# Performance work log

Hardware: AMD Instinct MI355X
Metric: run time of the kernel (lower is better)

The kernel has to match this reference:

```python
import jax, jax.numpy as jnp
import numpy as np

B, N, D, H = 2, 4096, 768, 12
HD = D // H  # head_dim = 64


def setup_inputs() -> dict:
    key = jax.random.key(0)
    k1, k2, k3, k4 = jax.random.split(key, 4)
    s = 1.0 / np.sqrt(D)
    return {
        "x": jax.random.normal(k1, (B, N, D), dtype=jnp.float32),
        "W_kqv": jax.random.normal(k2, (H, D, 3 * HD), dtype=jnp.float32) * s,
        "W_proj": jax.random.normal(k3, (D, D), dtype=jnp.float32) * s,
        "b_proj": jax.random.normal(k4, (D,), dtype=jnp.float32) * 0.02,
    }


def reference(x, W_kqv, W_proj, b_proj):
    # Per-head fused KQV projection: [B,N,D] x [H,D,3*HD] -> [B,H,N,3*HD]
    kqv = jnp.einsum("bnd,hde->bhne", x, W_kqv)
    # split order in source: k, q, v
    k, q, v = jnp.split(kqv, 3, axis=-1)  # each [B,H,N,HD]
    scale = 1.0 / np.sqrt(HD)
    scores = jnp.einsum("bhqd,bhkd->bhqk", q, k) * scale  # [B,H,N,N]
    causal = jnp.tril(jnp.ones((N, N), dtype=bool))
    scores = jnp.where(causal, scores, -jnp.inf)
    probs = jax.nn.softmax(scores, axis=-1)
    out = jnp.einsum("bhqk,bhkd->bhqd", probs, v)  # [B,H,N,HD]
    # concat heads along feature dim -> [B,N,D]
    out = out.transpose(0, 2, 1, 3).reshape(B, N, D)
    # output projection (dropout_rate=0.0 -> identity)
    return out @ W_proj.T + b_proj
```

## Files before the change

kernel.cpp:

```cpp
#include <hip/hip_runtime.h>

typedef _Float16 half8 __attribute__((ext_vector_type(8)));
typedef __fp16 fp16x2 __attribute__((ext_vector_type(2)));
typedef float floatx4 __attribute__((ext_vector_type(4)));
typedef float floatx16 __attribute__((ext_vector_type(16)));

#define MFMA_F16(a, b, c) __builtin_amdgcn_mfma_f32_16x16x32_f16((a), (b), (c), 0, 0, 0)
#define MFMA32(a, b, c) __builtin_amdgcn_mfma_f32_32x32x16_f16((a), (b), (c), 0, 0, 0)

__device__ __forceinline__ unsigned short f2h_bits(float f) {
    union { _Float16 h; unsigned short u; } cv;
    cv.h = (_Float16)f;
    return cv.u;
}

__device__ __forceinline__ unsigned pkrtz(float a, float b) {
    union { fp16x2 h; unsigned u; } cv;
    cv.h = __builtin_amdgcn_cvt_pkrtz(a, b);
    return cv.u;
}

__device__ __forceinline__ void swap32(unsigned a, unsigned b, int hi32,
                                       unsigned& r0, unsigned& r1) {
#if __has_builtin(__builtin_amdgcn_permlane32_swap)
    auto r = __builtin_amdgcn_permlane32_swap((int)a, (int)b, false, false);
    r0 = (unsigned)r[0];
    r1 = (unsigned)r[1];
#else
    unsigned ax = (unsigned)__shfl_xor((int)a, 32, 64);
    unsigned bx = (unsigned)__shfl_xor((int)b, 32, 64);
    r0 = hi32 ? bx : a;
    r1 = hi32 ? b : ax;
#endif
}

__device__ __forceinline__ float xhalf_max(float x) {
#if __has_builtin(__builtin_amdgcn_permlane32_swap)
    auto r = __builtin_amdgcn_permlane32_swap(__float_as_int(x), __float_as_int(x), false, false);
    return fmaxf(__int_as_float(r[0]), __int_as_float(r[1]));
#else
    return fmaxf(x, __shfl_xor(x, 32, 64));
#endif
}
__device__ __forceinline__ float xhalf_add(float x) {
#if __has_builtin(__builtin_amdgcn_permlane32_swap)
    auto r = __builtin_amdgcn_permlane32_swap(__float_as_int(x), __float_as_int(x), false, false);
    return __int_as_float(r[0]) + __int_as_float(r[1]);
#else
    return x + __shfl_xor(x, 32, 64);
#endif
}

__global__ void conv_x_kernel(const float* __restrict__ x, unsigned short* __restrict__ xb) {
    int i = blockIdx.x * 256 + threadIdx.x;
    float4 v = ((const float4*)x)[i];
    ushort4 o;
    o.x = f2h_bits(v.x); o.y = f2h_bits(v.y); o.z = f2h_bits(v.z); o.w = f2h_bits(v.w);
    ((ushort4*)xb)[i] = o;
}

__global__ void conv_wkqv_kernel(const float* __restrict__ w, unsigned short* __restrict__ wT) {
    int t = blockIdx.x * 256 + threadIdx.x;
    int d = t % 768;
    int hc = t / 768;
    int h = hc / 192;
    int c = hc - h * 192;
    float v = w[(h * 768 + d) * 192 + c];
    if (c >= 64 && c < 128) v *= 0.18033688011112042f;
    wT[t] = f2h_bits(v);
}

__global__ void conv_wproj_kernel(const float* __restrict__ w, unsigned short* __restrict__ wb) {
    int i = blockIdx.x * 256 + threadIdx.x;
    float4 v = ((const float4*)w)[i];
    ushort4 o;
    o.x = f2h_bits(v.x); o.y = f2h_bits(v.y); o.z = f2h_bits(v.z); o.w = f2h_bits(v.w);
    ((ushort4*)wb)[i] = o;
}

template <int EPI>
__global__ __launch_bounds__(256, 2) void gemm_bt_kernel(
    const unsigned short* __restrict__ A, const unsigned short* __restrict__ Bt,
    unsigned short* __restrict__ o_q, unsigned short* __restrict__ o_k,
    unsigned short* __restrict__ o_vt, float* __restrict__ o_f32,
    const float* __restrict__ bias, int Ntiles) {
    __shared__ unsigned short sA[128 * 64];
    __shared__ unsigned short sB[128 * 64];
    const int tid = threadIdx.x;
    const int lo = tid & 15;
    const int hi = (tid >> 4) & 3;
    const int wid = tid >> 6;
    const int wr = wid >> 1;
    const int wc = wid & 1;
    const int bm = blockIdx.x / Ntiles;
    const int bn = blockIdx.x % Ntiles;
    const size_t rowA0 = (size_t)bm * 128;
    const size_t rowB0 = (size_t)bn * 128;

    const floatx4 ZERO = {0.f, 0.f, 0.f, 0.f};
    floatx4 acc[4][4];
#pragma unroll
    for (int i = 0; i < 4; ++i)
#pragma unroll
        for (int j = 0; j < 4; ++j) acc[i][j] = ZERO;

    const int ldsWaveBase = (tid & 0xC0) << 3;

    for (int kt = 0; kt < 768; kt += 64) {
        __syncthreads();
#pragma unroll
        for (int it = 0; it < 4; ++it) {
            int g = it * 256 + tid;
            int row = g >> 3;
            int slot = g & 7;
            int koff = kt + ((slot ^ (row & 7)) << 3);
            const unsigned short* srcA = A + (rowA0 + row) * 768 + koff;
            const unsigned short* srcB = Bt + (rowB0 + row) * 768 + koff;
            unsigned short* dA = &sA[it * 2048 + ldsWaveBase];
            unsigned short* dB = &sB[it * 2048 + ldsWaveBase];
            __builtin_amdgcn_global_load_lds(
                (const __attribute__((address_space(1))) unsigned int*)srcA,
                (__attribute__((address_space(3))) unsigned int*)dA, 16, 0, 0);
            __builtin_amdgcn_global_load_lds(
                (const __attribute__((address_space(1))) unsigned int*)srcB,
                (__attribute__((address_space(3))) unsigned int*)dB, 16, 0, 0);
        }
        __syncthreads();
#pragma unroll
        for (int kc = 0; kc < 2; ++kc) {
            half8 av[4], bv[4];
#pragma unroll
            for (int mi = 0; mi < 4; ++mi) {
                int row = wr * 64 + mi * 16 + lo;
                av[mi] = *(const half8*)&sA[row * 64 + (((kc * 4 + hi) ^ (lo & 7)) << 3)];
            }
#pragma unroll
            for (int ni = 0; ni < 4; ++ni) {
                int row = wc * 64 + ni * 16 + lo;
                bv[ni] = *(const half8*)&sB[row * 64 + (((kc * 4 + hi) ^ (lo & 7)) << 3)];
            }
#pragma unroll
            for (int mi = 0; mi < 4; ++mi)
#pragma unroll
                for (int ni = 0; ni < 4; ++ni)
                    acc[mi][ni] = MFMA_F16(av[mi], bv[ni], acc[mi][ni]);
        }
    }

    if (EPI == 0) {
#pragma unroll
        for (int ni = 0; ni < 4; ++ni) {
            int gn = (int)rowB0 + wc * 64 + ni * 16 + lo;
            unsigned h = (unsigned)gn / 192u;
            int c = gn - (int)h * 192;
#pragma unroll
            for (int mi = 0; mi < 4; ++mi) {
#pragma unroll
                for (int r = 0; r < 4; ++r) {
                    int gm = (int)rowA0 + wr * 64 + mi * 16 + hi * 4 + r;
                    int b = gm >> 12;
                    int n = gm & 4095;
                    int bh = b * 12 + (int)h;
                    unsigned short val = f2h_bits(acc[mi][ni][r]);
                    if (c < 64) {
                        int t = n >> 5;
                        size_t idx = ((((size_t)bh * 128 + t) * 4 + (c >> 4)) * 64 +
                                      (((c >> 3) & 1) * 32 + (n & 31))) * 8 + (c & 7);
                        o_k[idx] = val;
                    } else if (c < 128) {
                        int d = c - 64;
                        int t = n >> 5;
                        size_t idx = ((((size_t)bh * 128 + t) * 4 + (d >> 4)) * 64 +
                                      (((d >> 3) & 1) * 32 + (n & 31))) * 8 + (d & 7);
                        o_q[idx] = val;
                    } else {
                        int dv = c - 128;
                        int t = n >> 5;
                        int kin = n & 31;
                        size_t idx = ((((size_t)bh * 128 + t) * 4 +
                                       ((dv >> 5) * 2 + (kin >> 4))) * 64 +
                                      (((kin >> 3) & 1) * 32 + (dv & 31))) * 8 + (kin & 7);
                        o_vt[idx] = val;
                    }
                }
            }
        }
    } else {
#pragma unroll
        for (int mi = 0; mi < 4; ++mi)
#pragma unroll
            for (int ni = 0; ni < 4; ++ni) {
                int gn = (int)rowB0 + wc * 64 + ni * 16 + lo;
                float bs = bias[gn];
#pragma unroll
                for (int r = 0; r < 4; ++r) {
                    int gm = (int)rowA0 + wr * 64 + mi * 16 + hi * 4 + r;
                    o_f32[(size_t)gm * 768 + gn] = acc[mi][ni][r] + bs;
                }
            }
    }
}

__global__ __launch_bounds__(128, 3) void attn_kernel(
    const unsigned short* __restrict__ Qw, const unsigned short* __restrict__ Kw,
    const unsigned short* __restrict__ Vtw, unsigned short* __restrict__ Ow) {
    __shared__ float sM[64 * 35];
    const int tid = threadIdx.x;
    const int lane = tid & 63;
    const int wid = tid >> 6;
    const int l31 = lane & 31;
    const int hi32 = lane >> 5;
    const int bh = blockIdx.x % 24;
    const int p = blockIdx.x / 24;
    const int b = bh / 12;
    const int h = bh - b * 12;

    const unsigned short* QF = Qw + (size_t)bh * 262144;
    const unsigned short* KF = Kw + (size_t)bh * 262144;
    const unsigned short* VF = Vtw + (size_t)bh * 262144;

    const floatx16 Z16 = {0.f,0.f,0.f,0.f,0.f,0.f,0.f,0.f,0.f,0.f,0.f,0.f,0.f,0.f,0.f,0.f};

    for (int pass = 0; pass < 2; ++pass) {
        const int band = pass ? 127 - p : p;
        const int q0 = band << 5;
        const int myq = q0 + l31;
        const int nk = (band >> 1) + 1;

        half8 qf[4];
#pragma unroll
        for (int ds = 0; ds < 4; ++ds)
            qf[ds] = *(const half8*)&QF[(((size_t)band * 4 + ds) * 64 + lane) * 8];

        floatx16 accO0 = Z16, accO1 = Z16;
        float mI = -1e30f, lI = 0.f;

        for (int i = wid; i < nk; i += 2) {
            const int kt = i << 6;
            const unsigned short* kb = &KF[(size_t)(2 * i) * 2048 + lane * 8];
            half8 kfa[4], kfb[4];
#pragma unroll
            for (int ds = 0; ds < 4; ++ds) {
                kfa[ds] = *(const half8*)(kb + ds * 512);
                kfb[ds] = *(const half8*)(kb + 2048 + ds * 512);
            }
            const unsigned short* vb0 = &VF[(size_t)(2 * i) * 2048 + lane * 8];
            half8 vf0[2][2], vf1[2][2];
#pragma unroll
            for (int dt = 0; dt < 2; ++dt)
#pragma unroll
                for (int j = 0; j < 2; ++j) {
                    vf0[dt][j] = *(const half8*)(vb0 + (dt * 2 + j) * 512);
                    vf1[dt][j] = *(const half8*)(vb0 + 2048 + (dt * 2 + j) * 512);
                }

            floatx16 s0 = Z16, s1 = Z16;
            __builtin_amdgcn_s_setprio(1);
#pragma unroll
            for (int ds = 0; ds < 4; ++ds) s0 = MFMA32(kfa[ds], qf[ds], s0);
#pragma unroll
            for (int ds = 0; ds < 4; ++ds) s1 = MFMA32(kfb[ds], qf[ds], s1);
            __builtin_amdgcn_s_setprio(0);

            if (i == nk - 1) {
#pragma unroll
                for (int r = 0; r < 16; ++r) {
                    int crow = (r & 3) + ((r >> 2) << 3) + (hi32 << 2);
                    if (kt + crow > myq) s0[r] = -1e30f;
                    if (kt + 32 + crow > myq) s1[r] = -1e30f;
                }
            }

            float ma[8];
#pragma unroll
            for (int r = 0; r < 8; ++r)
                ma[r] = fmaxf(fmaxf(s0[2 * r], s0[2 * r + 1]),
                              fmaxf(s1[2 * r], s1[2 * r + 1]));
            float mx = fmaxf(fmaxf(fmaxf(ma[0], ma[1]), fmaxf(ma[2], ma[3])),
                             fmaxf(fmaxf(ma[4], ma[5]), fmaxf(ma[6], ma[7])));
            mx = xhalf_max(mx);

            if (!__all(mx <= mI + 8.0f)) {
                float mn = fmaxf(mI, mx);
                float sc = exp2f(mI - mn);
                mI = mn;
                lI *= sc;
#pragma unroll
                for (int r = 0; r < 16; ++r) {
                    int src = (r & 3) + ((r >> 2) << 3) + (hi32 << 2);
                    float scb = __int_as_float(
                        __builtin_amdgcn_ds_bpermute(src << 2, __float_as_int(sc)));
                    accO0[r] *= scb;
                    accO1[r] *= scb;
                }
            }

#pragma unroll
            for (int r = 0; r < 16; ++r) {
                s0[r] = exp2f(s0[r] - mI);
                s1[r] = exp2f(s1[r] - mI);
            }
            float sa[8];
#pragma unroll
            for (int r = 0; r < 8; ++r)
                sa[r] = (s0[2 * r] + s0[2 * r + 1]) + (s1[2 * r] + s1[2 * r + 1]);
            float ps = ((sa[0] + sa[1]) + (sa[2] + sa[3])) +
                       ((sa[4] + sa[5]) + (sa[6] + sa[7]));
            lI += xhalf_add(ps);

            {
                unsigned pA0 = pkrtz(s0[0], s0[1]),   pA1 = pkrtz(s0[2], s0[3]);
                unsigned pB0 = pkrtz(s0[4], s0[5]),   pB1 = pkrtz(s0[6], s0[7]);
                unsigned pC0 = pkrtz(s0[8], s0[9]),   pC1 = pkrtz(s0[10], s0[11]);
                unsigned pD0 = pkrtz(s0[12], s0[13]), pD1 = pkrtz(s0[14], s0[15]);
                unsigned w0, w1, w2, w3, u0, u1, u2, u3;
                swap32(pA0, pB0, hi32, w0, w2);
                swap32(pA1, pB1, hi32, w1, w3);
                swap32(pC0, pD0, hi32, u0, u2);
                swap32(pC1, pD1, hi32, u1, u3);
                union { unsigned u[4]; half8 h; } f0, f1;
                f0.u[0] = w0; f0.u[1] = w1; f0.u[2] = w2; f0.u[3] = w3;
                f1.u[0] = u0; f1.u[1] = u1; f1.u[2] = u2; f1.u[3] = u3;
                __builtin_amdgcn_s_setprio(1);
                accO0 = MFMA32(f0.h, vf0[0][0], accO0);
                accO0 = MFMA32(f1.h, vf0[0][1], accO0);
                accO1 = MFMA32(f0.h, vf0[1][0], accO1);
                accO1 = MFMA32(f1.h, vf0[1][1], accO1);
                __builtin_amdgcn_s_setprio(0);
            }
            {
                unsigned pA0 = pkrtz(s1[0], s1[1]),   pA1 = pkrtz(s1[2], s1[3]);
                unsigned pB0 = pkrtz(s1[4], s1[5]),   pB1 = pkrtz(s1[6], s1[7]);
                unsigned pC0 = pkrtz(s1[8], s1[9]),   pC1 = pkrtz(s1[10], s1[11]);
                unsigned pD0 = pkrtz(s1[12], s1[13]), pD1 = pkrtz(s1[14], s1[15]);
                unsigned w0, w1, w2, w3, u0, u1, u2, u3;
                swap32(pA0, pB0, hi32, w0, w2);
                swap32(pA1, pB1, hi32, w1, w3);
                swap32(pC0, pD0, hi32, u0, u2);
                swap32(pC1, pD1, hi32, u1, u3);
                union { unsigned u[4]; half8 h; } f0, f1;
                f0.u[0] = w0; f0.u[1] = w1; f0.u[2] = w2; f0.u[3] = w3;
                f1.u[0] = u0; f1.u[1] = u1; f1.u[2] = u2; f1.u[3] = u3;
                __builtin_amdgcn_s_setprio(1);
                accO0 = MFMA32(f0.h, vf1[0][0], accO0);
                accO0 = MFMA32(f1.h, vf1[0][1], accO0);
                accO1 = MFMA32(f0.h, vf1[1][0], accO1);
                accO1 = MFMA32(f1.h, vf1[1][1], accO1);
                __builtin_amdgcn_s_setprio(0);
            }
        }

        if (wid == 1) {
            float* dst = &sM[lane * 35];
            dst[0] = mI;
            dst[1] = lI;
#pragma unroll
            for (int r = 0; r < 16; ++r) { dst[2 + r] = accO0[r]; dst[18 + r] = accO1[r]; }
        }
        __syncthreads();
        if (wid == 0) {
            const float* src = &sM[lane * 35];
            float m1 = src[0], l1 = src[1];
            float mstar = fmaxf(mI, m1);
            float sc0 = exp2f(mI - mstar);
            float sc1 = exp2f(m1 - mstar);
            float lt = lI * sc0 + l1 * sc1;
            float inv = 1.0f / lt;
            float f0 = sc0 * inv, f1 = sc1 * inv;
#pragma unroll
            for (int r = 0; r < 16; ++r) {
                int crow = (r & 3) + ((r >> 2) << 3) + (hi32 << 2);
                float fb0 = __int_as_float(
                    __builtin_amdgcn_ds_bpermute(crow << 2, __float_as_int(f0)));
                float fb1 = __int_as_float(
                    __builtin_amdgcn_ds_bpermute(crow << 2, __float_as_int(f1)));
                float o0 = accO0[r] * fb0 + src[2 + r] * fb1;
                float o1 = accO1[r] * fb0 + src[18 + r] * fb1;
                int qrow = q0 + crow;
                size_t base = ((size_t)(b * 4096 + qrow)) * 768 + h * 64;
                Ow[base + l31] = f2h_bits(o0);
                Ow[base + 32 + l31] = f2h_bits(o1);
            }
        }
        __syncthreads();
    }
}

extern "C" void kernel_launch(void* const* d_in, const int* in_sizes, int n_in,
                              void* d_out, int out_size, void* d_ws, size_t ws_size,
                              hipStream_t stream) {
    const float* x = (const float*)d_in[0];
    const float* wkqv = (const float*)d_in[1];
    const float* wproj = (const float*)d_in[2];
    const float* bproj = (const float*)d_in[3];
    float* out = (float*)d_out;

    char* ws = (char*)d_ws;
    unsigned short* xb = (unsigned short*)(ws);
    unsigned short* wkqvT = (unsigned short*)(ws + 12582912);
    unsigned short* wprojB = (unsigned short*)(ws + 16121856);
    unsigned short* Qw = (unsigned short*)(ws + 17301504);
    unsigned short* Kw = (unsigned short*)(ws + 29884416);
    unsigned short* Vtw = (unsigned short*)(ws + 42467328);
    unsigned short* Ow = xb;
    if (ws_size < 55050240) return;

    conv_x_kernel<<<6144, 256, 0, stream>>>(x, xb);
    conv_wkqv_kernel<<<6912, 256, 0, stream>>>(wkqv, wkqvT);
    conv_wproj_kernel<<<576, 256, 0, stream>>>(wproj, wprojB);
    gemm_bt_kernel<0><<<64 * 18, 256, 0, stream>>>(xb, wkqvT, Qw, Kw, Vtw, nullptr, nullptr, 18);
    attn_kernel<<<1536, 128, 0, stream>>>(Qw, Kw, Vtw, Ow);
    gemm_bt_kernel<1><<<64 * 6, 256, 0, stream>>>(Ow, wprojB, nullptr, nullptr, nullptr, out, bproj, 6);
}
```

Before: 179.7 us.

## Split attention key loop across four waves with LDS reduction

The attention block grows from two to four wavefronts. Each wave handles every fourth 64-key tile of a 32-query band. The partial softmax state (max, sum, accumulators) is merged through shared memory in a four-way reduction, and each wave writes a quarter of the output rows. Exponentials now go through the hardware exp2 builtin instead of exp2f. The aim is more parallelism per band and better latency hiding, at the cost of more LDS, extra barriers and a heavier merge step.

```diff
diff --git a/kernel.cpp b/kernel.cpp
--- a/kernel.cpp
+++ b/kernel.cpp
@@ -12,6 +12,14 @@
     union { _Float16 h; unsigned short u; } cv;
     cv.h = (_Float16)f;
     return cv.u;
+}
+
+__device__ __forceinline__ float exp2_hw(float x) {
+#if __has_builtin(__builtin_amdgcn_exp2f)
+    return __builtin_amdgcn_exp2f(x);
+#else
+    return exp2f(x);
+#endif
 }
 
 __device__ __forceinline__ unsigned pkrtz(float a, float b) {
@@ -49,6 +57,10 @@
 #else
     return x + __shfl_xor(x, 32, 64);
 #endif
+}
+
+__device__ __forceinline__ float bperm_f(int srclane, float v) {
+    return __int_as_float(__builtin_amdgcn_ds_bpermute(srclane << 2, __float_as_int(v)));
 }
 
 __global__ void conv_x_kernel(const float* __restrict__ x, unsigned short* __restrict__ xb) {
@@ -201,10 +213,12 @@
     }
 }
 
-__global__ __launch_bounds__(128, 3) void attn_kernel(
+__global__ __launch_bounds__(256, 4) void attn_kernel(
     const unsigned short* __restrict__ Qw, const unsigned short* __restrict__ Kw,
     const unsigned short* __restrict__ Vtw, unsigned short* __restrict__ Ow) {
-    __shared__ float sM[64 * 35];
+    __shared__ float sAcc[4 * 64 * 33];
+    __shared__ float sMl[4 * 64];
+    __shared__ float sLw[4 * 32];
     const int tid = threadIdx.x;
     const int lane = tid & 63;
     const int wid = tid >> 6;
@@ -235,7 +249,7 @@
         floatx16 accO0 = Z16, accO1 = Z16;
         float mI = -1e30f, lI = 0.f;
 
-        for (int i = wid; i < nk; i += 2) {
+        for (int i = wid; i < nk; i += 4) {
             const int kt = i << 6;
             const unsigned short* kb = &KF[(size_t)(2 * i) * 2048 + lane * 8];
             half8 kfa[4], kfb[4];
@@ -282,14 +296,13 @@
 
             if (!__all(mx <= mI + 8.0f)) {
                 float mn = fmaxf(mI, mx);
-                float sc = exp2f(mI - mn);
+                float sc = exp2_hw(mI - mn);
                 mI = mn;
                 lI *= sc;
 #pragma unroll
                 for (int r = 0; r < 16; ++r) {
                     int src = (r & 3) + ((r >> 2) << 3) + (hi32 << 2);
-                    float scb = __int_as_float(
-                        __builtin_amdgcn_ds_bpermute(src << 2, __float_as_int(sc)));
+                    float scb = bperm_f(src, sc);
                     accO0[r] *= scb;
                     accO1[r] *= scb;
                 }
@@ -297,8 +310,8 @@
 
 #pragma unroll
             for (int r = 0; r < 16; ++r) {
-                s0[r] = exp2f(s0[r] - mI);
-                s1[r] = exp2f(s1[r] - mI);
+                s0[r] = exp2_hw(s0[r] - mI);
+                s1[r] = exp2_hw(s1[r] - mI);
             }
             float sa[8];
 #pragma unroll
@@ -350,36 +363,38 @@
             }
         }
 
-        if (wid == 1) {
-            float* dst = &sM[lane * 35];
-            dst[0] = mI;
-            dst[1] = lI;
-#pragma unroll
-            for (int r = 0; r < 16; ++r) { dst[2 + r] = accO0[r]; dst[18 + r] = accO1[r]; }
-        }
+        sMl[wid * 64 + lane] = mI;
         __syncthreads();
-        if (wid == 0) {
-            const float* src = &sM[lane * 35];
-            float m1 = src[0], l1 = src[1];
-            float mstar = fmaxf(mI, m1);
-            float sc0 = exp2f(mI - mstar);
-            float sc1 = exp2f(m1 - mstar);
-            float lt = lI * sc0 + l1 * sc1;
-            float inv = 1.0f / lt;
-            float f0 = sc0 * inv, f1 = sc1 * inv;
+        float mstar = fmaxf(fmaxf(sMl[lane], sMl[64 + lane]),
+                            fmaxf(sMl[128 + lane], sMl[192 + lane]));
+        float f = exp2_hw(mI - mstar);
+        sLw[wid * 32 + l31] = lI * f;
+        {
+            float* slice = &sAcc[wid * 2112 + lane * 33];
 #pragma unroll
             for (int r = 0; r < 16; ++r) {
                 int crow = (r & 3) + ((r >> 2) << 3) + (hi32 << 2);
-                float fb0 = __int_as_float(
-                    __builtin_amdgcn_ds_bpermute(crow << 2, __float_as_int(f0)));
-                float fb1 = __int_as_float(
-                    __builtin_amdgcn_ds_bpermute(crow << 2, __float_as_int(f1)));
-                float o0 = accO0[r] * fb0 + src[2 + r] * fb1;
-                float o1 = accO1[r] * fb0 + src[18 + r] * fb1;
+                float fb = bperm_f(crow, f);
+                slice[r] = accO0[r] * fb;
+                slice[16 + r] = accO1[r] * fb;
+            }
+        }
+        __syncthreads();
+        {
+            float lsum = (sLw[l31] + sLw[32 + l31]) + (sLw[64 + l31] + sLw[96 + l31]);
+            float linv = 1.0f / lsum;
+            const float* base = &sAcc[lane * 33];
+#pragma unroll
+            for (int j = 0; j < 8; ++j) {
+                int r = wid * 8 + j;
+                int rr = r & 15;
+                int half = r >> 4;
+                float v = (base[r] + base[2112 + r]) + (base[4224 + r] + base[6336 + r]);
+                int crow = (rr & 3) + ((rr >> 2) << 3) + (hi32 << 2);
+                float lb = bperm_f(crow, linv);
                 int qrow = q0 + crow;
-                size_t base = ((size_t)(b * 4096 + qrow)) * 768 + h * 64;
-                Ow[base + l31] = f2h_bits(o0);
-                Ow[base + 32 + l31] = f2h_bits(o1);
+                Ow[((size_t)(b * 4096 + qrow)) * 768 + h * 64 + half * 32 + l31] =
+                    f2h_bits(v * lb);
             }
         }
         __syncthreads();
@@ -409,6 +424,6 @@
     conv_wkqv_kernel<<<6912, 256, 0, stream>>>(wkqv, wkqvT);
     conv_wproj_kernel<<<576, 256, 0, stream>>>(wproj, wprojB);
     gemm_bt_kernel<0><<<64 * 18, 256, 0, stream>>>(xb, wkqvT, Qw, Kw, Vtw, nullptr, nullptr, 18);
-    attn_kernel<<<1536, 128, 0, stream>>>(Qw, Kw, Vtw, Ow);
+    attn_kernel<<<1536, 256, 0, stream>>>(Qw, Kw, Vtw, Ow);
     gemm_bt_kernel<1><<<64 * 6, 256, 0, stream>>>(Ow, wprojB, nullptr, nullptr, nullptr, out, bproj, 6);
 }
```

Result: slower. 293.2 us (+63.2%).
